# Kernel tuning notes

Measured on AMD Instinct MI355X. Metric: run time of the kernel, lower is better.

## Reference

```python
import jax, jax.numpy as jnp
import numpy as np

B, H, S, D = 2, 12, 2048, 64

def setup_inputs() -> dict:
    key = jax.random.key(0)
    kq, kk, kv = jax.random.split(key, 3)
    Q = jax.random.normal(kq, (B, H, S, D), dtype=jnp.float32)
    K = jax.random.normal(kk, (B, H, S, D), dtype=jnp.float32)
    V = jax.random.normal(kv, (B, H, S, D), dtype=jnp.float32)
    return {"Q": Q, "K": K, "V": V}

def reference(Q, K, V):
    # NOTE: original code scales by sqrt(Q.shape[-2]) (the sequence length),
    # not the head dim — reproduced faithfully.
    scale = 1.0 / np.sqrt(Q.shape[-2]).astype(np.float32)
    scores = jnp.einsum('bhqd,bhkd->bhqk', Q, K) * scale  # [B,H,S,S]
    attn = jax.nn.softmax(scores, axis=-1)
    context = jnp.einsum('bhqk,bhkd->bhqd', attn, V)      # [B,H,S,D]
    # torch .squeeze(-1) only removes the last dim if it is size 1; D=64 so no-op
    return context
```

## Files before the change

### kernel.cpp

```cpp
#include <hip/hip_runtime.h>
#include <math.h>
#include <stdint.h>

#define BATCH 2
#define NH 12
#define SEQ 2048
#define HD 64
#define TQ 64
#define TK 64
#define NHEADS (BATCH*NH)

typedef short bf16x8 __attribute__((ext_vector_type(8)));
typedef float f32x4 __attribute__((ext_vector_type(4)));
typedef unsigned short us8_t __attribute__((ext_vector_type(8)));

#if __has_builtin(__builtin_amdgcn_exp2f)
#define EXP2F(x) __builtin_amdgcn_exp2f(x)
#else
#define EXP2F(x) exp2f(x)
#endif

static __device__ __forceinline__ unsigned short f2bf(float f) {
    unsigned int u = __float_as_uint(f);
    u += 0x7fffu + ((u >> 16) & 1u);
    return (unsigned short)(u >> 16);
}

static __device__ __forceinline__ void async_cp16(const void* g, void* l) {
    __builtin_amdgcn_global_load_lds(
        (const __attribute__((address_space(1))) void*)g,
        (__attribute__((address_space(3))) void*)(uintptr_t)l,
        16, 0, 0);
}

__global__ __launch_bounds__(256)
void cvt_qk(const float* __restrict__ Q, const float* __restrict__ K,
            unsigned short* __restrict__ Qb, unsigned short* __restrict__ Kb,
            float qs) {
    const int half = (NHEADS * SEQ * HD) / 8;
    int idx = blockIdx.x * 256 + threadIdx.x;
    const float* src; unsigned short* dst; float s;
    if (idx < half) { src = Q; dst = Qb; s = qs; }
    else            { src = K; dst = Kb; s = 1.0f; idx -= half; }
    const int e0 = idx * 8;
    float4 a = *(const float4*)&src[e0];
    float4 b = *(const float4*)&src[e0 + 4];
    us8_t r = { f2bf(a.x*s), f2bf(a.y*s), f2bf(a.z*s), f2bf(a.w*s),
                f2bf(b.x*s), f2bf(b.y*s), f2bf(b.z*s), f2bf(b.w*s) };
    *(us8_t*)&dst[e0] = r;
}

__global__ __launch_bounds__(256)
void vtrans(const float* __restrict__ V, unsigned short* __restrict__ Vtb) {
    __shared__ unsigned short T[64][65];
    const int bh = blockIdx.x >> 5;
    const int s0 = (blockIdx.x & 31) * 64;
    const int tid = threadIdx.x;
    const float* Vh = V + (size_t)bh * SEQ * HD;
    #pragma unroll
    for (int i = 0; i < 4; ++i) {
        int idx = tid + 256 * i;
        int row = idx >> 4;
        int c4  = (idx & 15) * 4;
        float4 v = *(const float4*)&Vh[(size_t)(s0 + row) * HD + c4];
        T[row][c4+0] = f2bf(v.x); T[row][c4+1] = f2bf(v.y);
        T[row][c4+2] = f2bf(v.z); T[row][c4+3] = f2bf(v.w);
    }
    __syncthreads();
    unsigned short* Vth = Vtb + (size_t)bh * HD * SEQ;
    #pragma unroll
    for (int i = 0; i < 2; ++i) {
        int idx = tid + 256 * i;
        int d  = idx >> 3;
        int ch = idx & 7;
        us8_t r;
        #pragma unroll
        for (int j = 0; j < 8; ++j) r[j] = T[ch*8 + j][d];
        *(us8_t*)&Vth[(size_t)d * SEQ + s0 + ch*8] = r;
    }
}

__global__ __launch_bounds__(256, 4)
void fa_main(const unsigned short* __restrict__ Qb,
             const unsigned short* __restrict__ Kb,
             const unsigned short* __restrict__ Vtb,
             float* __restrict__ O) {
    const int x  = blockIdx.x & 7;
    const int t  = blockIdx.x >> 3;
    const int bh = x + 8 * (t % 3);
    const int qt = t / 3;
    const int q0 = qt * TQ;

    __shared__ unsigned short Qs[TQ * HD];
    __shared__ unsigned short Ks[TK * HD];
    __shared__ unsigned short Vs[HD * TK];
    __shared__ unsigned short Ps[TQ][TK + 8];
    __shared__ float Lp[4][TQ];

    const int tid   = threadIdx.x;
    const int w     = tid >> 6;
    const int lane  = tid & 63;
    const int col   = lane & 15;
    const int quad  = lane >> 4;
    const int rloc  = lane >> 3;
    const int cphys = lane & 7;
    const int swz   = col & 7;

    const unsigned short* Qh = Qb  + (size_t)bh * SEQ * HD;
    const unsigned short* Kh = Kb  + (size_t)bh * SEQ * HD;
    const unsigned short* Vh = Vtb + (size_t)bh * HD * SEQ;

    {
        const int R = w * 16;
        async_cp16(Qh + (size_t)(q0 + R     + rloc) * HD + (cphys ^ rloc) * 8, &Qs[ R      * HD]);
        async_cp16(Qh + (size_t)(q0 + R + 8 + rloc) * HD + (cphys ^ rloc) * 8, &Qs[(R + 8) * HD]);
    }
    __syncthreads();

    bf16x8 aq[4][2];
    #pragma unroll
    for (int mt = 0; mt < 4; ++mt) {
        aq[mt][0] = *(const bf16x8*)&Qs[(mt*16 + col) * HD + ((quad     ^ swz) * 8)];
        aq[mt][1] = *(const bf16x8*)&Qs[(mt*16 + col) * HD + (((quad+4) ^ swz) * 8)];
    }

    f32x4 o[4];
    #pragma unroll
    for (int mt = 0; mt < 4; ++mt) o[mt] = (f32x4){0.f, 0.f, 0.f, 0.f};
    float lsum[4][4];
    #pragma unroll
    for (int mt = 0; mt < 4; ++mt)
        #pragma unroll
        for (int r = 0; r < 4; ++r) lsum[mt][r] = 0.f;

    for (int kv0 = 0; kv0 < SEQ; kv0 += TK) {
        __syncthreads();
        {
            const int R = w * 16;
            async_cp16(Kh + (size_t)(kv0 + R     + rloc) * HD  + (cphys ^ rloc) * 8, &Ks[ R      * HD]);
            async_cp16(Kh + (size_t)(kv0 + R + 8 + rloc) * HD  + (cphys ^ rloc) * 8, &Ks[(R + 8) * HD]);
            async_cp16(Vh + (size_t)(R     + rloc) * SEQ + kv0 + (cphys ^ rloc) * 8, &Vs[ R      * TK]);
            async_cp16(Vh + (size_t)(R + 8 + rloc) * SEQ + kv0 + (cphys ^ rloc) * 8, &Vs[(R + 8) * TK]);
        }
        __syncthreads();

        const int brow = w * 16 + col;
        bf16x8 bk0 = *(const bf16x8*)&Ks[brow * HD + ((quad     ^ swz) * 8)];
        bf16x8 bk1 = *(const bf16x8*)&Ks[brow * HD + (((quad+4) ^ swz) * 8)];
        f32x4 sc[4];
        #pragma unroll
        for (int mt = 0; mt < 4; ++mt) {
            f32x4 z = {0.f, 0.f, 0.f, 0.f};
            z = __builtin_amdgcn_mfma_f32_16x16x32_bf16(aq[mt][0], bk0, z, 0, 0, 0);
            z = __builtin_amdgcn_mfma_f32_16x16x32_bf16(aq[mt][1], bk1, z, 0, 0, 0);
            sc[mt] = z;
        }

        #pragma unroll
        for (int mt = 0; mt < 4; ++mt) {
            #pragma unroll
            for (int r = 0; r < 4; ++r) {
                float p = EXP2F(sc[mt][r]);
                lsum[mt][r] += p;
                Ps[mt*16 + quad*4 + r][w*16 + col] = f2bf(p);
            }
        }
        __syncthreads();

        bf16x8 bv0 = *(const bf16x8*)&Vs[brow * TK + ((quad     ^ swz) * 8)];
        bf16x8 bv1 = *(const bf16x8*)&Vs[brow * TK + (((quad+4) ^ swz) * 8)];
        #pragma unroll
        for (int mt = 0; mt < 4; ++mt) {
            bf16x8 ap0 = *(const bf16x8*)&Ps[mt*16 + col][quad * 8];
            bf16x8 ap1 = *(const bf16x8*)&Ps[mt*16 + col][32 + quad * 8];
            o[mt] = __builtin_amdgcn_mfma_f32_16x16x32_bf16(ap0, bv0, o[mt], 0, 0, 0);
            o[mt] = __builtin_amdgcn_mfma_f32_16x16x32_bf16(ap1, bv1, o[mt], 0, 0, 0);
        }
    }

    #pragma unroll
    for (int off = 1; off < 16; off <<= 1)
        #pragma unroll
        for (int mt = 0; mt < 4; ++mt)
            #pragma unroll
            for (int r = 0; r < 4; ++r)
                lsum[mt][r] += __shfl_xor(lsum[mt][r], off, 64);
    if (col == 0) {
        #pragma unroll
        for (int mt = 0; mt < 4; ++mt)
            #pragma unroll
            for (int r = 0; r < 4; ++r)
                Lp[w][mt*16 + quad*4 + r] = lsum[mt][r];
    }
    __syncthreads();

    float* Oh = O + (size_t)bh * SEQ * HD + (size_t)q0 * HD;
    #pragma unroll
    for (int mt = 0; mt < 4; ++mt) {
        #pragma unroll
        for (int r = 0; r < 4; ++r) {
            int row = mt*16 + quad*4 + r;
            float l = Lp[0][row] + Lp[1][row] + Lp[2][row] + Lp[3][row];
            Oh[(size_t)row * HD + w*16 + col] = o[mt][r] * (1.0f / l);
        }
    }
}

#define PAD 8
#define LSTR (HD + PAD)

__global__ __launch_bounds__(256)
void fa_fwd_fb(const float* __restrict__ Q, const float* __restrict__ K,
               const float* __restrict__ V, float* __restrict__ O) {
    const int x  = blockIdx.x & 7;
    const int t  = blockIdx.x >> 3;
    const int bh = x + 8 * (t % 3);
    const int qt = t / 3;
    const int q0 = qt * TQ;
    const long base = (long)bh * SEQ * HD;

    __shared__ unsigned short Qs[TQ][LSTR];
    __shared__ unsigned short Ks2[TK][LSTR];
    __shared__ unsigned short Vt[HD][TK + PAD];
    __shared__ unsigned short Ps2[4][16][LSTR];

    const int tid  = threadIdx.x;
    const int wave = tid >> 6;
    const int lane = tid & 63;
    const int col  = lane & 15;
    const int quad = lane >> 4;
    const int m0   = wave * 16;

    #pragma unroll
    for (int i = 0; i < 4; ++i) {
        int idx = tid + 256 * i;
        int row = idx >> 4;
        int c4  = (idx & 15) * 4;
        float4 v = *(const float4*)&Q[base + (long)(q0 + row) * HD + c4];
        ushort4 b = { f2bf(v.x), f2bf(v.y), f2bf(v.z), f2bf(v.w) };
        *(ushort4*)&Qs[row][c4] = b;
    }
    __syncthreads();

    bf16x8 aq0 = *(const bf16x8*)&Qs[m0 + col][quad * 8];
    bf16x8 aq1 = *(const bf16x8*)&Qs[m0 + col][32 + quad * 8];

    f32x4 o0 = {0.f,0.f,0.f,0.f}, o1 = o0, o2 = o0, o3 = o0;
    float l[4] = {0.f, 0.f, 0.f, 0.f};
    const float scale = 0.022097086912079608f;

    for (int kv0 = 0; kv0 < SEQ; kv0 += TK) {
        __syncthreads();
        #pragma unroll
        for (int i = 0; i < 4; ++i) {
            int idx = tid + 256 * i;
            int row = idx >> 4;
            int c4  = (idx & 15) * 4;
            float4 kv = *(const float4*)&K[base + (long)(kv0 + row) * HD + c4];
            ushort4 kb = { f2bf(kv.x), f2bf(kv.y), f2bf(kv.z), f2bf(kv.w) };
            *(ushort4*)&Ks2[row][c4] = kb;
            float4 vv = *(const float4*)&V[base + (long)(kv0 + row) * HD + c4];
            Vt[c4 + 0][row] = f2bf(vv.x);
            Vt[c4 + 1][row] = f2bf(vv.y);
            Vt[c4 + 2][row] = f2bf(vv.z);
            Vt[c4 + 3][row] = f2bf(vv.w);
        }
        __syncthreads();

        f32x4 sc[4];
        #pragma unroll
        for (int n = 0; n < 4; ++n) {
            bf16x8 b0 = *(const bf16x8*)&Ks2[n * 16 + col][quad * 8];
            bf16x8 b1 = *(const bf16x8*)&Ks2[n * 16 + col][32 + quad * 8];
            f32x4 acc = {0.f,0.f,0.f,0.f};
            acc = __builtin_amdgcn_mfma_f32_16x16x32_bf16(aq0, b0, acc, 0, 0, 0);
            acc = __builtin_amdgcn_mfma_f32_16x16x32_bf16(aq1, b1, acc, 0, 0, 0);
            sc[n] = acc;
        }

        float tsum[4] = {0.f, 0.f, 0.f, 0.f};
        #pragma unroll
        for (int n = 0; n < 4; ++n) {
            #pragma unroll
            for (int r = 0; r < 4; ++r) {
                float p = __expf(sc[n][r] * scale);
                tsum[r] += p;
                Ps2[wave][quad * 4 + r][n * 16 + col] = f2bf(p);
            }
        }
        #pragma unroll
        for (int off = 1; off < 16; off <<= 1) {
            #pragma unroll
            for (int r = 0; r < 4; ++r) tsum[r] += __shfl_xor(tsum[r], off, 64);
        }
        #pragma unroll
        for (int r = 0; r < 4; ++r) l[r] += tsum[r];

        bf16x8 ap0 = *(const bf16x8*)&Ps2[wave][col][quad * 8];
        bf16x8 ap1 = *(const bf16x8*)&Ps2[wave][col][32 + quad * 8];
        #pragma unroll
        for (int n = 0; n < 4; ++n) {
            bf16x8 b0 = *(const bf16x8*)&Vt[n * 16 + col][quad * 8];
            bf16x8 b1 = *(const bf16x8*)&Vt[n * 16 + col][32 + quad * 8];
            f32x4* op = (n == 0) ? &o0 : (n == 1) ? &o1 : (n == 2) ? &o2 : &o3;
            *op = __builtin_amdgcn_mfma_f32_16x16x32_bf16(ap0, b0, *op, 0, 0, 0);
            *op = __builtin_amdgcn_mfma_f32_16x16x32_bf16(ap1, b1, *op, 0, 0, 0);
        }
    }

    float inv[4];
    #pragma unroll
    for (int r = 0; r < 4; ++r) inv[r] = 1.0f / l[r];
    #pragma unroll
    for (int r = 0; r < 4; ++r) {
        long row = base + (long)(q0 + m0 + quad * 4 + r) * HD;
        O[row +  0 + col] = o0[r] * inv[r];
        O[row + 16 + col] = o1[r] * inv[r];
        O[row + 32 + col] = o2[r] * inv[r];
        O[row + 48 + col] = o3[r] * inv[r];
    }
}

extern "C" void kernel_launch(void* const* d_in, const int* in_sizes, int n_in,
                              void* d_out, int out_size, void* d_ws, size_t ws_size,
                              hipStream_t stream) {
    const float* Q = (const float*)d_in[0];
    const float* K = (const float*)d_in[1];
    const float* V = (const float*)d_in[2];
    float* O = (float*)d_out;

    const size_t tensorElems = (size_t)NHEADS * SEQ * HD;
    const size_t need = 3 * tensorElems * sizeof(unsigned short);

    if (ws_size >= need) {
        unsigned short* Qb  = (unsigned short*)d_ws;
        unsigned short* Kb  = Qb + tensorElems;
        unsigned short* Vtb = Kb + tensorElems;
        const float qs = (float)(1.4426950408889634 / sqrt(2048.0));
        cvt_qk<<<dim3(2 * tensorElems / 8 / 256), dim3(256), 0, stream>>>(Q, K, Qb, Kb, qs);
        vtrans<<<dim3(NHEADS * (SEQ / 64)), dim3(256), 0, stream>>>(V, Vtb);
        fa_main<<<dim3(NHEADS * (SEQ / TQ)), dim3(256), 0, stream>>>(Qb, Kb, Vtb, O);
    } else {
        fa_fwd_fb<<<dim3(NHEADS * (SEQ / TQ)), dim3(256), 0, stream>>>(Q, K, V, O);
    }
}
```

Measured before the change: 132.7 us.

## Double-buffer K/V tiles, split warps by query rows, fuse Q conversion and prep kernels

Each warp now owns 16 query rows instead of 16 key columns. Softmax sums and the P tile therefore stay per-warp, which removes the cross-warp reduction and one block barrier per iteration. K/V tiles are double-buffered with async global-to-LDS loads that prefetch the next tile while the current one is computed. Q is converted to bf16 and scaled inside the main kernel, and the K-convert and V-transpose prep kernels are merged into one launch. The risks are that the V transpose now uses scattered 2-byte stores and that the launch-bounds occupancy hint was dropped, so the larger LDS footprint may reduce occupancy.

```diff
diff --git a/kernel.cpp b/kernel.cpp
--- a/kernel.cpp
+++ b/kernel.cpp
@@ -9,6 +9,7 @@
 #define TQ 64
 #define TK 64
 #define NHEADS (BATCH*NH)
+#define NIT (SEQ / TK)
 
 typedef short bf16x8 __attribute__((ext_vector_type(8)));
 typedef float f32x4 __attribute__((ext_vector_type(4)));
@@ -34,57 +35,44 @@
 }
 
 __global__ __launch_bounds__(256)
-void cvt_qk(const float* __restrict__ Q, const float* __restrict__ K,
-            unsigned short* __restrict__ Qb, unsigned short* __restrict__ Kb,
-            float qs) {
-    const int half = (NHEADS * SEQ * HD) / 8;
-    int idx = blockIdx.x * 256 + threadIdx.x;
-    const float* src; unsigned short* dst; float s;
-    if (idx < half) { src = Q; dst = Qb; s = qs; }
-    else            { src = K; dst = Kb; s = 1.0f; idx -= half; }
-    const int e0 = idx * 8;
-    float4 a = *(const float4*)&src[e0];
-    float4 b = *(const float4*)&src[e0 + 4];
-    us8_t r = { f2bf(a.x*s), f2bf(a.y*s), f2bf(a.z*s), f2bf(a.w*s),
-                f2bf(b.x*s), f2bf(b.y*s), f2bf(b.z*s), f2bf(b.w*s) };
-    *(us8_t*)&dst[e0] = r;
-}
-
-__global__ __launch_bounds__(256)
-void vtrans(const float* __restrict__ V, unsigned short* __restrict__ Vtb) {
-    __shared__ unsigned short T[64][65];
+void prep_kv(const float* __restrict__ K, const float* __restrict__ V,
+             unsigned short* __restrict__ Kb, unsigned short* __restrict__ Vtb) {
     const int bh = blockIdx.x >> 5;
     const int s0 = (blockIdx.x & 31) * 64;
     const int tid = threadIdx.x;
-    const float* Vh = V + (size_t)bh * SEQ * HD;
+
+    const float* Ksrc = K + ((size_t)bh * SEQ + s0) * HD;
+    unsigned short* Kdst = Kb + ((size_t)bh * SEQ + s0) * HD;
+    #pragma unroll
+    for (int i = 0; i < 2; ++i) {
+        int e0 = (tid + 256 * i) * 8;
+        float4 a = *(const float4*)&Ksrc[e0];
+        float4 b = *(const float4*)&Ksrc[e0 + 4];
+        us8_t r = { f2bf(a.x), f2bf(a.y), f2bf(a.z), f2bf(a.w),
+                    f2bf(b.x), f2bf(b.y), f2bf(b.z), f2bf(b.w) };
+        *(us8_t*)&Kdst[e0] = r;
+    }
+
+    const float* Vsrc = V + ((size_t)bh * SEQ + s0) * HD;
+    unsigned short* Vdst = Vtb + (size_t)bh * HD * SEQ;
+    const int n  = tid & 63;
+    const int cg = tid >> 6;
     #pragma unroll
     for (int i = 0; i < 4; ++i) {
-        int idx = tid + 256 * i;
-        int row = idx >> 4;
-        int c4  = (idx & 15) * 4;
-        float4 v = *(const float4*)&Vh[(size_t)(s0 + row) * HD + c4];
-        T[row][c4+0] = f2bf(v.x); T[row][c4+1] = f2bf(v.y);
-        T[row][c4+2] = f2bf(v.z); T[row][c4+3] = f2bf(v.w);
-    }
-    __syncthreads();
-    unsigned short* Vth = Vtb + (size_t)bh * HD * SEQ;
-    #pragma unroll
-    for (int i = 0; i < 2; ++i) {
-        int idx = tid + 256 * i;
-        int d  = idx >> 3;
-        int ch = idx & 7;
-        us8_t r;
-        #pragma unroll
-        for (int j = 0; j < 8; ++j) r[j] = T[ch*8 + j][d];
-        *(us8_t*)&Vth[(size_t)d * SEQ + s0 + ch*8] = r;
-    }
-}
-
-__global__ __launch_bounds__(256, 4)
-void fa_main(const unsigned short* __restrict__ Qb,
+        int c4 = (cg + 4 * i) * 4;
+        float4 v = *(const float4*)&Vsrc[(size_t)n * HD + c4];
+        Vdst[(size_t)(c4 + 0) * SEQ + s0 + n] = f2bf(v.x);
+        Vdst[(size_t)(c4 + 1) * SEQ + s0 + n] = f2bf(v.y);
+        Vdst[(size_t)(c4 + 2) * SEQ + s0 + n] = f2bf(v.z);
+        Vdst[(size_t)(c4 + 3) * SEQ + s0 + n] = f2bf(v.w);
+    }
+}
+
+__global__ __launch_bounds__(256)
+void fa_main(const float* __restrict__ Q,
              const unsigned short* __restrict__ Kb,
              const unsigned short* __restrict__ Vtb,
-             float* __restrict__ O) {
+             float* __restrict__ O, float qs) {
     const int x  = blockIdx.x & 7;
     const int t  = blockIdx.x >> 3;
     const int bh = x + 8 * (t % 3);
@@ -92,10 +80,9 @@
     const int q0 = qt * TQ;
 
     __shared__ unsigned short Qs[TQ * HD];
-    __shared__ unsigned short Ks[TK * HD];
-    __shared__ unsigned short Vs[HD * TK];
-    __shared__ unsigned short Ps[TQ][TK + 8];
-    __shared__ float Lp[4][TQ];
+    __shared__ unsigned short Kdb[2][TK * HD];
+    __shared__ unsigned short Vdb[2][HD * TK];
+    __shared__ unsigned short Ps[4][16][72];
 
     const int tid   = threadIdx.x;
     const int w     = tid >> 6;
@@ -105,104 +92,107 @@
     const int rloc  = lane >> 3;
     const int cphys = lane & 7;
     const int swz   = col & 7;
-
-    const unsigned short* Qh = Qb  + (size_t)bh * SEQ * HD;
+    const int R     = w * 16;
+
+    const float*          Qh = Q   + ((size_t)bh * SEQ + q0) * HD;
     const unsigned short* Kh = Kb  + (size_t)bh * SEQ * HD;
     const unsigned short* Vh = Vtb + (size_t)bh * HD * SEQ;
 
+    #pragma unroll
+    for (int i = 0; i < 2; ++i) {
+        int c   = tid * 2 + i;
+        int row = c >> 3;
+        int ch  = c & 7;
+        const float* src = &Qh[(size_t)row * HD + ch * 8];
+        float4 a = *(const float4*)&src[0];
+        float4 b = *(const float4*)&src[4];
+        us8_t r = { f2bf(a.x*qs), f2bf(a.y*qs), f2bf(a.z*qs), f2bf(a.w*qs),
+                    f2bf(b.x*qs), f2bf(b.y*qs), f2bf(b.z*qs), f2bf(b.w*qs) };
+        *(us8_t*)&Qs[row * HD + ((ch ^ (row & 7)) * 8)] = r;
+    }
+
     {
-        const int R = w * 16;
-        async_cp16(Qh + (size_t)(q0 + R     + rloc) * HD + (cphys ^ rloc) * 8, &Qs[ R      * HD]);
-        async_cp16(Qh + (size_t)(q0 + R + 8 + rloc) * HD + (cphys ^ rloc) * 8, &Qs[(R + 8) * HD]);
+        async_cp16(Kh + (size_t)(0 + R     + rloc) * HD  + (cphys ^ rloc) * 8, &Kdb[0][ R      * HD]);
+        async_cp16(Kh + (size_t)(0 + R + 8 + rloc) * HD  + (cphys ^ rloc) * 8, &Kdb[0][(R + 8) * HD]);
+        async_cp16(Vh + (size_t)(R     + rloc) * SEQ + 0 + (cphys ^ rloc) * 8, &Vdb[0][ R      * TK]);
+        async_cp16(Vh + (size_t)(R + 8 + rloc) * SEQ + 0 + (cphys ^ rloc) * 8, &Vdb[0][(R + 8) * TK]);
     }
     __syncthreads();
 
-    bf16x8 aq[4][2];
-    #pragma unroll
-    for (int mt = 0; mt < 4; ++mt) {
-        aq[mt][0] = *(const bf16x8*)&Qs[(mt*16 + col) * HD + ((quad     ^ swz) * 8)];
-        aq[mt][1] = *(const bf16x8*)&Qs[(mt*16 + col) * HD + (((quad+4) ^ swz) * 8)];
-    }
+    bf16x8 aq0 = *(const bf16x8*)&Qs[(R + col) * HD + ((quad       ^ swz) * 8)];
+    bf16x8 aq1 = *(const bf16x8*)&Qs[(R + col) * HD + (((quad + 4) ^ swz) * 8)];
 
     f32x4 o[4];
     #pragma unroll
-    for (int mt = 0; mt < 4; ++mt) o[mt] = (f32x4){0.f, 0.f, 0.f, 0.f};
-    float lsum[4][4];
-    #pragma unroll
-    for (int mt = 0; mt < 4; ++mt)
-        #pragma unroll
-        for (int r = 0; r < 4; ++r) lsum[mt][r] = 0.f;
-
-    for (int kv0 = 0; kv0 < SEQ; kv0 += TK) {
-        __syncthreads();
-        {
-            const int R = w * 16;
-            async_cp16(Kh + (size_t)(kv0 + R     + rloc) * HD  + (cphys ^ rloc) * 8, &Ks[ R      * HD]);
-            async_cp16(Kh + (size_t)(kv0 + R + 8 + rloc) * HD  + (cphys ^ rloc) * 8, &Ks[(R + 8) * HD]);
-            async_cp16(Vh + (size_t)(R     + rloc) * SEQ + kv0 + (cphys ^ rloc) * 8, &Vs[ R      * TK]);
-            async_cp16(Vh + (size_t)(R + 8 + rloc) * SEQ + kv0 + (cphys ^ rloc) * 8, &Vs[(R + 8) * TK]);
-        }
-        __syncthreads();
-
-        const int brow = w * 16 + col;
-        bf16x8 bk0 = *(const bf16x8*)&Ks[brow * HD + ((quad     ^ swz) * 8)];
-        bf16x8 bk1 = *(const bf16x8*)&Ks[brow * HD + (((quad+4) ^ swz) * 8)];
+    for (int nt = 0; nt < 4; ++nt) o[nt] = (f32x4){0.f, 0.f, 0.f, 0.f};
+    float lsum[4] = {0.f, 0.f, 0.f, 0.f};
+
+    for (int it = 0; it < NIT; ++it) {
+        const int cur = it & 1;
+        if (it + 1 < NIT) {
+            const int nb  = cur ^ 1;
+            const int kv0 = (it + 1) * TK;
+            async_cp16(Kh + (size_t)(kv0 + R     + rloc) * HD  + (cphys ^ rloc) * 8, &Kdb[nb][ R      * HD]);
+            async_cp16(Kh + (size_t)(kv0 + R + 8 + rloc) * HD  + (cphys ^ rloc) * 8, &Kdb[nb][(R + 8) * HD]);
+            async_cp16(Vh + (size_t)(R     + rloc) * SEQ + kv0 + (cphys ^ rloc) * 8, &Vdb[nb][ R      * TK]);
+            async_cp16(Vh + (size_t)(R + 8 + rloc) * SEQ + kv0 + (cphys ^ rloc) * 8, &Vdb[nb][(R + 8) * TK]);
+        }
+        const unsigned short* Ks = Kdb[cur];
+        const unsigned short* Vs = Vdb[cur];
+
         f32x4 sc[4];
         #pragma unroll
-        for (int mt = 0; mt < 4; ++mt) {
+        for (int nt = 0; nt < 4; ++nt) {
+            const int br = nt * 16 + col;
+            bf16x8 bk0 = *(const bf16x8*)&Ks[br * HD + ((quad       ^ swz) * 8)];
+            bf16x8 bk1 = *(const bf16x8*)&Ks[br * HD + (((quad + 4) ^ swz) * 8)];
             f32x4 z = {0.f, 0.f, 0.f, 0.f};
-            z = __builtin_amdgcn_mfma_f32_16x16x32_bf16(aq[mt][0], bk0, z, 0, 0, 0);
-            z = __builtin_amdgcn_mfma_f32_16x16x32_bf16(aq[mt][1], bk1, z, 0, 0, 0);
-            sc[mt] = z;
-        }
-
-        #pragma unroll
-        for (int mt = 0; mt < 4; ++mt) {
+            z = __builtin_amdgcn_mfma_f32_16x16x32_bf16(aq0, bk0, z, 0, 0, 0);
+            z = __builtin_amdgcn_mfma_f32_16x16x32_bf16(aq1, bk1, z, 0, 0, 0);
+            sc[nt] = z;
+        }
+
+        #pragma unroll
+        for (int nt = 0; nt < 4; ++nt) {
             #pragma unroll
             for (int r = 0; r < 4; ++r) {
-                float p = EXP2F(sc[mt][r]);
-                lsum[mt][r] += p;
-                Ps[mt*16 + quad*4 + r][w*16 + col] = f2bf(p);
+                float p = EXP2F(sc[nt][r]);
+                lsum[r] += p;
+                Ps[w][quad * 4 + r][nt * 16 + col] = f2bf(p);
             }
         }
+
+        bf16x8 ap0 = *(const bf16x8*)&Ps[w][col][quad * 8];
+        bf16x8 ap1 = *(const bf16x8*)&Ps[w][col][32 + quad * 8];
+        #pragma unroll
+        for (int nt = 0; nt < 4; ++nt) {
+            const int br = nt * 16 + col;
+            bf16x8 bv0 = *(const bf16x8*)&Vs[br * TK + ((quad       ^ swz) * 8)];
+            bf16x8 bv1 = *(const bf16x8*)&Vs[br * TK + (((quad + 4) ^ swz) * 8)];
+            o[nt] = __builtin_amdgcn_mfma_f32_16x16x32_bf16(ap0, bv0, o[nt], 0, 0, 0);
+            o[nt] = __builtin_amdgcn_mfma_f32_16x16x32_bf16(ap1, bv1, o[nt], 0, 0, 0);
+        }
+
         __syncthreads();
-
-        bf16x8 bv0 = *(const bf16x8*)&Vs[brow * TK + ((quad     ^ swz) * 8)];
-        bf16x8 bv1 = *(const bf16x8*)&Vs[brow * TK + (((quad+4) ^ swz) * 8)];
-        #pragma unroll
-        for (int mt = 0; mt < 4; ++mt) {
-            bf16x8 ap0 = *(const bf16x8*)&Ps[mt*16 + col][quad * 8];
-            bf16x8 ap1 = *(const bf16x8*)&Ps[mt*16 + col][32 + quad * 8];
-            o[mt] = __builtin_amdgcn_mfma_f32_16x16x32_bf16(ap0, bv0, o[mt], 0, 0, 0);
-            o[mt] = __builtin_amdgcn_mfma_f32_16x16x32_bf16(ap1, bv1, o[mt], 0, 0, 0);
-        }
     }
 
     #pragma unroll
     for (int off = 1; off < 16; off <<= 1)
         #pragma unroll
-        for (int mt = 0; mt < 4; ++mt)
-            #pragma unroll
-            for (int r = 0; r < 4; ++r)
-                lsum[mt][r] += __shfl_xor(lsum[mt][r], off, 64);
-    if (col == 0) {
-        #pragma unroll
-        for (int mt = 0; mt < 4; ++mt)
-            #pragma unroll
-            for (int r = 0; r < 4; ++r)
-                Lp[w][mt*16 + quad*4 + r] = lsum[mt][r];
-    }
-    __syncthreads();
-
-    float* Oh = O + (size_t)bh * SEQ * HD + (size_t)q0 * HD;
-    #pragma unroll
-    for (int mt = 0; mt < 4; ++mt) {
-        #pragma unroll
-        for (int r = 0; r < 4; ++r) {
-            int row = mt*16 + quad*4 + r;
-            float l = Lp[0][row] + Lp[1][row] + Lp[2][row] + Lp[3][row];
-            Oh[(size_t)row * HD + w*16 + col] = o[mt][r] * (1.0f / l);
-        }
+        for (int r = 0; r < 4; ++r) lsum[r] += __shfl_xor(lsum[r], off, 64);
+
+    float inv[4];
+    #pragma unroll
+    for (int r = 0; r < 4; ++r) inv[r] = 1.0f / lsum[r];
+
+    float* Oh = O + ((size_t)bh * SEQ + q0) * HD;
+    #pragma unroll
+    for (int r = 0; r < 4; ++r) {
+        size_t row = (size_t)(R + quad * 4 + r) * HD;
+        Oh[row +  0 + col] = o[0][r] * inv[r];
+        Oh[row + 16 + col] = o[1][r] * inv[r];
+        Oh[row + 32 + col] = o[2][r] * inv[r];
+        Oh[row + 48 + col] = o[3][r] * inv[r];
     }
 }
 
@@ -330,16 +320,14 @@
     float* O = (float*)d_out;
 
     const size_t tensorElems = (size_t)NHEADS * SEQ * HD;
-    const size_t need = 3 * tensorElems * sizeof(unsigned short);
+    const size_t need = 2 * tensorElems * sizeof(unsigned short);
 
     if (ws_size >= need) {
-        unsigned short* Qb  = (unsigned short*)d_ws;
-        unsigned short* Kb  = Qb + tensorElems;
+        unsigned short* Kb  = (unsigned short*)d_ws;
         unsigned short* Vtb = Kb + tensorElems;
         const float qs = (float)(1.4426950408889634 / sqrt(2048.0));
-        cvt_qk<<<dim3(2 * tensorElems / 8 / 256), dim3(256), 0, stream>>>(Q, K, Qb, Kb, qs);
-        vtrans<<<dim3(NHEADS * (SEQ / 64)), dim3(256), 0, stream>>>(V, Vtb);
-        fa_main<<<dim3(NHEADS * (SEQ / TQ)), dim3(256), 0, stream>>>(Qb, Kb, Vtb, O);
+        prep_kv<<<dim3(NHEADS * (SEQ / 64)), dim3(256), 0, stream>>>(K, V, Kb, Vtb);
+        fa_main<<<dim3(NHEADS * (SEQ / TQ)), dim3(256), 0, stream>>>(Q, Kb, Vtb, O, qs);
     } else {
         fa_fwd_fb<<<dim3(NHEADS * (SEQ / TQ)), dim3(256), 0, stream>>>(Q, K, V, O);
     }
```

Result: no change. 130.5 us (-1.6%).
